# Kernel optimization log

Measured on AMD Instinct MI355X. Metric: run time of the kernel, lower is better.

## Reference

```python
import jax, jax.numpy as jnp
import numpy as np
from jax import lax

SIZES = [(159, 159), (159, 159), (79, 79), (79, 79), (39, 39), (19, 19), (19, 19), (19, 19)]
STRIDES = [4, 4, 8, 8, 16, 32, 32, 32]
RF_SIZES = [55.0, 71.0, 111.0, 143.0, 223.0, 383.0, 511.0, 639.0]
SCORE_THR = 0.35
IOU_THR = 0.5
MAX_BOXES = 100
BATCH = 32
CLS_C = 3  # class_num + 1


def _coords_fmap2orig(size, stride):
    h, w = size
    ys = (jnp.arange(h, dtype=jnp.float32) * stride + stride / 2.0)
    xs = (jnp.arange(w, dtype=jnp.float32) * stride + stride / 2.0)
    X, Y = jnp.meshgrid(xs, ys)  # row-major over (h, w)
    return jnp.stack([X.reshape(-1), Y.reshape(-1)], axis=-1)  # [h*w, 2]


def _flatten_cat(branches):
    # each branch [b,c,h,w] -> [b,h*w,c]; concat over anchors
    outs = [x.transpose(0, 2, 3, 1).reshape(x.shape[0], -1, x.shape[1]) for x in branches]
    return jnp.concatenate(outs, axis=1)


def _nms_keep(boxes, valid):
    # boxes [K,4] sorted by score desc, valid [K] bool. Greedy NMS, +1 area convention.
    x1, y1, x2, y2 = boxes[:, 0], boxes[:, 1], boxes[:, 2], boxes[:, 3]
    areas = (x2 - x1 + 1.0) * (y2 - y1 + 1.0)
    xmin = jnp.maximum(x1[:, None], x1[None, :])
    ymin = jnp.maximum(y1[:, None], y1[None, :])
    xmax = jnp.minimum(x2[:, None], x2[None, :])
    ymax = jnp.minimum(y2[:, None], y2[None, :])
    inter = jnp.clip(xmax - xmin, 0.0) * jnp.clip(ymax - ymin, 0.0)
    iou = inter / (areas[:, None] + areas[None, :] - inter)
    idx = jnp.arange(boxes.shape[0])

    def body(i, keep):
        sup = (iou[i] > IOU_THR) & (idx > i) & keep[i]
        return keep & ~sup

    return lax.fori_loop(0, boxes.shape[0], body, valid)


def setup_inputs() -> dict:
    key = jax.random.key(0)
    inp = {}
    ks = jax.random.split(key, 16)
    for i, (h, w) in enumerate(SIZES):
        inp[f"cls{i}"] = jax.random.normal(ks[i], (BATCH, CLS_C, h, w), dtype=jnp.float32)
        inp[f"reg{i}"] = jax.random.normal(ks[8 + i], (BATCH, 4, h, w), dtype=jnp.float32)
    return inp


def reference(cls0, cls1, cls2, cls3, cls4, cls5, cls6, cls7,
              reg0, reg1, reg2, reg3, reg4, reg5, reg6, reg7):
    cls_branches = [cls0, cls1, cls2, cls3, cls4, cls5, cls6, cls7]
    reg_branches = [reg0, reg1, reg2, reg3, reg4, reg5, reg6, reg7]

    cls_logits = _flatten_cat(cls_branches)   # [B, N, 3]
    reg_preds = _flatten_cat(reg_branches)    # [B, N, 4]
    coords = jnp.concatenate([_coords_fmap2orig(s, st) for s, st in zip(SIZES, STRIDES)], axis=0)  # [N,2]

    cls_preds = jax.nn.softmax(cls_logits, axis=2)
    cls_scores = jnp.max(cls_preds, axis=2)      # [B,N]
    cls_classes = jnp.argmax(cls_preds, axis=2)  # [B,N]

    rf_scale = jnp.concatenate([
        jnp.full((h * w,), rf / 2.0, dtype=jnp.float32) for (h, w), rf in zip(SIZES, RF_SIZES)
    ])  # [N]
    reg_preds = reg_preds * rf_scale[None, :, None]
    x1y1 = coords[None, :, :] - reg_preds[..., :2]
    x2y2 = coords[None, :, :] + reg_preds[..., 2:]
    boxes = jnp.concatenate([x1y1, x2y2], axis=2)  # [B,N,4]

    # foreground mask -> mask scores so topk picks fg first
    fg = cls_classes > 0
    masked_scores = jnp.where(fg, cls_scores, -1.0)
    top_scores, top_idx = lax.top_k(masked_scores, MAX_BOXES)  # [B,K], sorted desc
    top_boxes = jnp.take_along_axis(boxes, top_idx[..., None], axis=1)      # [B,K,4]
    top_classes = jnp.take_along_axis(cls_classes, top_idx, axis=1)         # [B,K]

    valid = (top_scores >= SCORE_THR) & (top_classes > 0)
    keep = jax.vmap(_nms_keep)(top_boxes, valid)  # [B,K] bool

    out_scores = jnp.where(keep, top_scores, 0.0)
    out_classes = jnp.where(keep, top_classes, 0)
    out_boxes = jnp.where(keep[..., None], top_boxes, 0.0)
    return out_scores, out_classes, out_boxes, keep
```

## Files before the change

kernel.cpp:

```cpp
#include <hip/hip_runtime.h>
#include <stdint.h>

#define N_ANCH 65648
#define NCHUNK 65
#define CHUNK  1024
#define NQ16   4103
#define CAP    2048
#define KBASE  0xBE800000u
#define NBATCH 32
#define TOPK   100
#define FT     1024

struct Ptrs { const float* cls[8]; const float* reg[8]; };

__constant__ int   c_off[9] = {0,25281,50562,56803,63044,64565,64926,65287,65648};
__constant__ int   c_sz[8]  = {159,159,79,79,39,19,19,19};
__constant__ float c_st[8]  = {4.f,4.f,8.f,8.f,16.f,32.f,32.f,32.f};
__constant__ float c_rf[8]  = {27.5f,35.5f,55.5f,71.5f,111.5f,191.5f,255.5f,319.5f};

__device__ inline uint32_t anchor_key(const Ptrs& p, int b, int n) {
  int k = 0;
#pragma unroll
  for (int q = 1; q < 8; ++q) if (n >= c_off[q]) k = q;
  int local = n - c_off[k];
  int hw = c_sz[k] * c_sz[k];
  const float* c = p.cls[k] + (size_t)(b * 3) * hw + local;
  float l0 = c[0], l1 = c[(size_t)hw], l2 = c[(size_t)2 * hw];
  float m = l0; int cl = 0;
  if (l1 > m) { m = l1; cl = 1; }
  if (l2 > m) { m = l2; cl = 2; }
  if (cl == 0) return 0u;
  float s = 1.0f / (expf(l0 - m) + expf(l1 - m) + expf(l2 - m));
  return __float_as_uint(s) | 0x80000000u;
}

__global__ __launch_bounds__(256) void k_bins(Ptrs p, uint8_t* bins, uint16_t* hist) {
  int bid = blockIdx.x;
  int b = bid / NCHUNK, chunk = bid % NCHUNK;
  int t = threadIdx.x;
  __shared__ uint32_t lh[256];
  lh[t] = 0;
  __syncthreads();
  int n0 = chunk * CHUNK + t * 4;
  if (n0 < N_ANCH) {
    uchar4 v; uint8_t* vb = (uint8_t*)&v;
#pragma unroll
    for (int u = 0; u < 4; ++u) {
      uint32_t key = anchor_key(p, b, n0 + u);
      uint8_t bin = key ? (uint8_t)((key - KBASE) >> 16) : (uint8_t)0;
      vb[u] = bin;
      if (bin) atomicAdd(&lh[bin], 1u);
    }
    *(uchar4*)(bins + (size_t)b * N_ANCH + n0) = v;
  }
  __syncthreads();
  hist[((size_t)b * NCHUNK + chunk) * 256 + t] = (uint16_t)lh[t];
}

template<int U>
__device__ inline void rank_select(const unsigned long long* s_all, int c, int c8, int t,
                                   unsigned long long* top) {
  unsigned long long mine[U]; int rk[U];
#pragma unroll
  for (int u = 0; u < U; ++u) {
    int i = t + u * FT;
    mine[u] = (i < c) ? s_all[i] : 0ull;
    rk[u] = 0;
  }
  for (int j = 0; j < c8; j += 8) {
    unsigned long long v0 = s_all[j+0], v1 = s_all[j+1], v2 = s_all[j+2], v3 = s_all[j+3];
    unsigned long long v4 = s_all[j+4], v5 = s_all[j+5], v6 = s_all[j+6], v7 = s_all[j+7];
#pragma unroll
    for (int u = 0; u < U; ++u) {
      rk[u] += (v0 > mine[u]) + (v1 > mine[u]) + (v2 > mine[u]) + (v3 > mine[u])
             + (v4 > mine[u]) + (v5 > mine[u]) + (v6 > mine[u]) + (v7 > mine[u]);
    }
  }
#pragma unroll
  for (int u = 0; u < U; ++u) {
    int i = t + u * FT;
    if (i < c && rk[u] < TOPK) top[rk[u]] = mine[u];
  }
}

__global__ __launch_bounds__(FT) void k_sel(Ptrs p, const uint8_t* bins,
                                            const uint16_t* hist, float* out) {
  int b = blockIdx.x, t = threadIdx.x;
  __shared__ uint32_t part[4][256];
  __shared__ uint32_t tot[256];
  __shared__ int s_idx[CAP];
  __shared__ unsigned long long s_all[CAP + 8];
  __shared__ unsigned long long top[TOPK];
  __shared__ float bx1[TOPK], by1[TOPK], bx2[TOPK], by2[TOPK], area[TOPK], sc[TOPK];
  __shared__ int cls_s[TOPK], keep[TOPK];
  __shared__ unsigned long long sup0[TOPK], sup1[TOPK];
  __shared__ unsigned long long s_km[2], s_km2[2];
  __shared__ uint32_t s_cnt;
  __shared__ int s_thr;

  {
    const uint16_t* hb = hist + (size_t)b * NCHUNK * 256;
    int g = t >> 8, tb = t & 255;
    uint32_t v0 = 0, v1 = 0, v2 = 0, v3 = 0;
    for (int ch = g; ch < NCHUNK; ch += 16) {
      v0 += hb[ch * 256 + tb];
      if (ch + 4 < NCHUNK)  v1 += hb[(ch + 4) * 256 + tb];
      if (ch + 8 < NCHUNK)  v2 += hb[(ch + 8) * 256 + tb];
      if (ch + 12 < NCHUNK) v3 += hb[(ch + 12) * 256 + tb];
    }
    part[g][tb] = v0 + v1 + v2 + v3;
    if (t == 0) s_cnt = 0;
    if (t < TOPK) top[t] = 0ull;
    __syncthreads();
    if (t < 256) tot[t] = part[0][t] + part[1][t] + part[2][t] + part[3][t];
    __syncthreads();
    for (int d = 1; d < 256; d <<= 1) {
      uint32_t add = 0;
      if (t < 256 && t + d < 256) add = tot[t + d];
      __syncthreads();
      if (t < 256) tot[t] += add;
      __syncthreads();
    }
    if (t < 256) {
      uint32_t suf = tot[t], sufn = (t < 255) ? tot[t + 1] : 0u;
      if (suf >= TOPK && sufn < TOPK) s_thr = t;
      if (t == 0 && tot[0] < TOPK) s_thr = 0;
    }
    __syncthreads();
  }
  int thr = s_thr; if (thr < 1) thr = 1;

  {
    const uint4* bp = (const uint4*)(bins + (size_t)b * N_ANCH);
    for (int i = t; i < NQ16; i += FT) {
      uint4 v4 = bp[i];
      uint32_t ws[4] = { v4.x, v4.y, v4.z, v4.w };
#pragma unroll
      for (int w = 0; w < 4; ++w) {
        uint32_t wv = ws[w];
        if (!wv) continue;
#pragma unroll
        for (int u = 0; u < 4; ++u) {
          int bin = (wv >> (8 * u)) & 0xFF;
          if (bin >= thr) {
            uint32_t q = atomicAdd(&s_cnt, 1u);
            if (q < CAP) s_idx[q] = i * 16 + w * 4 + u;
          }
        }
      }
    }
  }
  __syncthreads();
  int c = (int)min(s_cnt, (uint32_t)CAP);
  int c8 = (c + 7) & ~7;

  for (int i = t; i < c; i += FT) {
    int n = s_idx[i];
    s_all[i] = ((unsigned long long)anchor_key(p, b, n) << 32) | (uint32_t)(~(uint32_t)n);
  }
  for (int i = c + t; i < c8; i += FT) s_all[i] = 0ull;
  __syncthreads();

  if (c <= FT) rank_select<1>(s_all, c, c8, t, top);
  else         rank_select<2>(s_all, c, c8, t, top);
  __syncthreads();

  if (t < TOPK) {
    int r = t;
    unsigned long long pk = top[r];
    if (pk == 0ull) {
      sc[r] = -1.f; cls_s[r] = 0; keep[r] = 0;
      bx1[r] = by1[r] = bx2[r] = by2[r] = 0.f; area[r] = 1.f;
    } else {
      uint32_t key = (uint32_t)(pk >> 32);
      int n = (int)(~(uint32_t)pk);
      float score = __uint_as_float(key & 0x7FFFFFFFu);
      int k2 = 0;
#pragma unroll
      for (int q = 1; q < 8; ++q) if (n >= c_off[q]) k2 = q;
      int local = n - c_off[k2];
      int w = c_sz[k2], hw = w * w;
      int i2 = local / w, j2 = local % w;
      const float* cp = p.cls[k2] + (size_t)(b * 3) * hw + local;
      float l0 = cp[0], l1 = cp[(size_t)hw], l2 = cp[(size_t)2 * hw];
      float m = l0; int cl = 0;
      if (l1 > m) { m = l1; cl = 1; }
      if (l2 > m) { m = l2; cl = 2; }
      const float* rp = p.reg[k2] + (size_t)(b * 4) * hw + local;
      float r0 = rp[0], r1 = rp[(size_t)hw], r2 = rp[(size_t)2 * hw], r3 = rp[(size_t)3 * hw];
      float st = c_st[k2], rf = c_rf[k2];
      float cx = (float)j2 * st + st * 0.5f;
      float cy = (float)i2 * st + st * 0.5f;
      float x1 = cx - r0 * rf, y1 = cy - r1 * rf;
      float x2 = cx + r2 * rf, y2 = cy + r3 * rf;
      sc[r] = score; cls_s[r] = cl;
      bx1[r] = x1; by1[r] = y1; bx2[r] = x2; by2[r] = y2;
      area[r] = (x2 - x1 + 1.0f) * (y2 - y1 + 1.0f);
      keep[r] = (score >= 0.35f && cl > 0) ? 1 : 0;
    }
  }
  __syncthreads();

  if (t < TOPK) {
    float a1x = bx1[t], a1y = by1[t], a2x = bx2[t], a2y = by2[t], aA = area[t];
    unsigned long long m0 = 0, m1 = 0;
    for (int j = t + 1; j < TOPK; ++j) {
      float xmin = fmaxf(a1x, bx1[j]), ymin = fmaxf(a1y, by1[j]);
      float xmax = fminf(a2x, bx2[j]), ymax = fminf(a2y, by2[j]);
      float inter = fmaxf(xmax - xmin, 0.f) * fmaxf(ymax - ymin, 0.f);
      float iou = inter / (aA + area[j] - inter);
      if (iou > 0.5f) { if (j < 64) m0 |= 1ull << j; else m1 |= 1ull << (j - 64); }
    }
    sup0[t] = m0; sup1[t] = m1;
  }
  if (t < 64) {
    unsigned long long m = __ballot(keep[t] != 0);
    if (t == 0) s_km[0] = m;
  } else if (t < 128) {
    unsigned long long m = __ballot(t < TOPK && keep[t] != 0);
    if (t == 64) s_km[1] = m;
  }
  __syncthreads();

  if (t == 0) {
    unsigned long long km0 = s_km[0], km1 = s_km[1];
    for (int i0 = 0; i0 < TOPK; i0 += 8) {
      unsigned long long a0[8], a1[8];
#pragma unroll
      for (int q = 0; q < 8; ++q) {
        int i = i0 + q;
        a0[q] = (i < TOPK) ? sup0[i] : 0ull;
        a1[q] = (i < TOPK) ? sup1[i] : 0ull;
      }
#pragma unroll
      for (int q = 0; q < 8; ++q) {
        int i = i0 + q;
        if (i < TOPK) {
          bool ki = (i < 64) ? ((km0 >> i) & 1) : ((km1 >> (i - 64)) & 1);
          if (ki) { km0 &= ~a0[q]; km1 &= ~a1[q]; }
        }
      }
    }
    s_km2[0] = km0; s_km2[1] = km1;
  }
  __syncthreads();

  if (t < TOPK) {
    int r = t, o = b * TOPK + r;
    bool kp = (r < 64) ? ((s_km2[0] >> r) & 1) : ((s_km2[1] >> (r - 64)) & 1);
    out[o] = kp ? sc[r] : 0.f;
    out[NBATCH * TOPK + o] = kp ? (float)cls_s[r] : 0.f;
    float* ob = out + 2 * NBATCH * TOPK + (size_t)o * 4;
    ob[0] = kp ? bx1[r] : 0.f;
    ob[1] = kp ? by1[r] : 0.f;
    ob[2] = kp ? bx2[r] : 0.f;
    ob[3] = kp ? by2[r] : 0.f;
    out[6 * NBATCH * TOPK + o] = kp ? 1.f : 0.f;
  }
}

extern "C" void kernel_launch(void* const* d_in, const int* in_sizes, int n_in,
                              void* d_out, int out_size, void* d_ws, size_t ws_size,
                              hipStream_t stream) {
  Ptrs p;
  for (int i = 0; i < 8; ++i) {
    p.cls[i] = (const float*)d_in[2 * i];
    p.reg[i] = (const float*)d_in[2 * i + 1];
  }
  uint8_t*  bins = (uint8_t*)d_ws;
  uint16_t* hist = (uint16_t*)((char*)d_ws + 2100736);
  float* out = (float*)d_out;

  k_bins<<<NBATCH * NCHUNK, 256, 0, stream>>>(p, bins, hist);
  k_sel<<<NBATCH, FT, 0, stream>>>(p, bins, hist, out);
}
```

Measured before the change: 49.16 us.

## Split candidate collection into per-chunk kernel before per-batch merge

Moves the histogram threshold search, bin scan and candidate key computation out of the 32-block selection kernel into a new kernel launched with one block per (batch, chunk). Each block writes its candidates to a workspace segment, and a merge kernel prefix-sums the per-chunk counts and gathers the segments before rank selection and NMS. The intent is to spread the serial scan and the gather of candidate keys over 2080 blocks instead of 32. The cost is an extra launch, each block redoing the 65-chunk histogram reduction, and a round trip through global memory for the candidate keys.

```diff
diff --git a/kernel.cpp b/kernel.cpp
--- a/kernel.cpp
+++ b/kernel.cpp
@@ -4,12 +4,12 @@
 #define N_ANCH 65648
 #define NCHUNK 65
 #define CHUNK  1024
-#define NQ16   4103
+#define SEGCAP 1024
 #define CAP    2048
 #define KBASE  0xBE800000u
 #define NBATCH 32
 #define TOPK   100
-#define FT     1024
+#define MT     1024
 
 struct Ptrs { const float* cls[8]; const float* reg[8]; };
 
@@ -57,112 +57,113 @@
   hist[((size_t)b * NCHUNK + chunk) * 256 + t] = (uint16_t)lh[t];
 }
 
-template<int U>
-__device__ inline void rank_select(const unsigned long long* s_all, int c, int c8, int t,
-                                   unsigned long long* top) {
-  unsigned long long mine[U]; int rk[U];
-#pragma unroll
-  for (int u = 0; u < U; ++u) {
-    int i = t + u * FT;
-    mine[u] = (i < c) ? s_all[i] : 0ull;
-    rk[u] = 0;
-  }
-  for (int j = 0; j < c8; j += 8) {
-    unsigned long long v0 = s_all[j+0], v1 = s_all[j+1], v2 = s_all[j+2], v3 = s_all[j+3];
-    unsigned long long v4 = s_all[j+4], v5 = s_all[j+5], v6 = s_all[j+6], v7 = s_all[j+7];
-#pragma unroll
-    for (int u = 0; u < U; ++u) {
-      rk[u] += (v0 > mine[u]) + (v1 > mine[u]) + (v2 > mine[u]) + (v3 > mine[u])
-             + (v4 > mine[u]) + (v5 > mine[u]) + (v6 > mine[u]) + (v7 > mine[u]);
-    }
-  }
-#pragma unroll
-  for (int u = 0; u < U; ++u) {
-    int i = t + u * FT;
-    if (i < c && rk[u] < TOPK) top[rk[u]] = mine[u];
-  }
-}
-
-__global__ __launch_bounds__(FT) void k_sel(Ptrs p, const uint8_t* bins,
-                                            const uint16_t* hist, float* out) {
+__global__ __launch_bounds__(256) void k_collect(Ptrs p, const uint8_t* bins,
+                                                 const uint16_t* hist,
+                                                 unsigned long long* seg, uint32_t* cnt) {
+  int bid = blockIdx.x;
+  int b = bid / NCHUNK, chunk = bid % NCHUNK;
+  int t = threadIdx.x;
+  __shared__ uint32_t tot[256];
+  __shared__ int s_thr;
+  __shared__ uint32_t s_cnt;
+
+  const uint16_t* hb = hist + (size_t)b * NCHUNK * 256;
+  {
+    uint32_t v0 = 0, v1 = 0, v2 = 0, v3 = 0;
+    int ch = 0;
+    for (; ch + 4 <= NCHUNK; ch += 4) {
+      v0 += hb[(ch + 0) * 256 + t];
+      v1 += hb[(ch + 1) * 256 + t];
+      v2 += hb[(ch + 2) * 256 + t];
+      v3 += hb[(ch + 3) * 256 + t];
+    }
+    for (; ch < NCHUNK; ++ch) v0 += hb[ch * 256 + t];
+    tot[t] = v0 + v1 + v2 + v3;
+    if (t == 0) s_cnt = 0;
+    __syncthreads();
+    for (int d = 1; d < 256; d <<= 1) {
+      uint32_t add = (t + d < 256) ? tot[t + d] : 0u;
+      __syncthreads();
+      tot[t] += add;
+      __syncthreads();
+    }
+    uint32_t suf = tot[t], sufn = (t < 255) ? tot[t + 1] : 0u;
+    if (suf >= TOPK && sufn < TOPK) s_thr = t;
+    if (t == 0 && tot[0] < TOPK) s_thr = 0;
+    __syncthreads();
+  }
+  int thr = s_thr; if (thr < 1) thr = 1;
+
+  int n0 = chunk * CHUNK + t * 4;
+  unsigned long long* sg = seg + (size_t)bid * SEGCAP;
+  if (n0 < N_ANCH) {
+    uchar4 v4 = *(const uchar4*)(bins + (size_t)b * N_ANCH + n0);
+    const uint8_t* vb = (const uint8_t*)&v4;
+#pragma unroll
+    for (int u = 0; u < 4; ++u) {
+      if (vb[u] >= thr) {
+        uint32_t pos = atomicAdd(&s_cnt, 1u);
+        int n = n0 + u;
+        sg[pos] = ((unsigned long long)anchor_key(p, b, n) << 32) |
+                  (uint32_t)(~(uint32_t)n);
+      }
+    }
+  }
+  __syncthreads();
+  if (t == 0) cnt[bid] = s_cnt;
+}
+
+__global__ __launch_bounds__(MT) void k_merge(Ptrs p, const uint32_t* cnt,
+                                              const unsigned long long* seg, float* out) {
   int b = blockIdx.x, t = threadIdx.x;
-  __shared__ uint32_t part[4][256];
-  __shared__ uint32_t tot[256];
-  __shared__ int s_idx[CAP];
+  __shared__ uint32_t pref[NCHUNK + 1];
   __shared__ unsigned long long s_all[CAP + 8];
   __shared__ unsigned long long top[TOPK];
   __shared__ float bx1[TOPK], by1[TOPK], bx2[TOPK], by2[TOPK], area[TOPK], sc[TOPK];
   __shared__ int cls_s[TOPK], keep[TOPK];
   __shared__ unsigned long long sup0[TOPK], sup1[TOPK];
   __shared__ unsigned long long s_km[2], s_km2[2];
-  __shared__ uint32_t s_cnt;
-  __shared__ int s_thr;
+
+  if (t < NCHUNK) pref[t + 1] = cnt[b * NCHUNK + t];
+  if (t == 0) pref[0] = 0;
+  if (t < TOPK) top[t] = 0ull;
+  __syncthreads();
+  for (int d = 1; d < NCHUNK + 1; d <<= 1) {
+    uint32_t v = 0;
+    if (t < NCHUNK + 1 && t >= d) v = pref[t - d];
+    __syncthreads();
+    if (t < NCHUNK + 1) pref[t] += v;
+    __syncthreads();
+  }
+  int c = (int)min(pref[NCHUNK], (uint32_t)CAP);
+  int c8 = (c + 7) & ~7;
+
+  for (int i = t; i < c; i += MT) {
+    int lo = 0, hi = NCHUNK - 1;
+    while (lo < hi) {
+      int mid = (lo + hi + 1) >> 1;
+      if ((int)pref[mid] <= i) lo = mid; else hi = mid - 1;
+    }
+    s_all[i] = seg[((size_t)b * NCHUNK + lo) * SEGCAP + (i - (int)pref[lo])];
+  }
+  for (int i = c + t; i < c8; i += MT) s_all[i] = 0ull;
+  __syncthreads();
 
   {
-    const uint16_t* hb = hist + (size_t)b * NCHUNK * 256;
-    int g = t >> 8, tb = t & 255;
-    uint32_t v0 = 0, v1 = 0, v2 = 0, v3 = 0;
-    for (int ch = g; ch < NCHUNK; ch += 16) {
-      v0 += hb[ch * 256 + tb];
-      if (ch + 4 < NCHUNK)  v1 += hb[(ch + 4) * 256 + tb];
-      if (ch + 8 < NCHUNK)  v2 += hb[(ch + 8) * 256 + tb];
-      if (ch + 12 < NCHUNK) v3 += hb[(ch + 12) * 256 + tb];
-    }
-    part[g][tb] = v0 + v1 + v2 + v3;
-    if (t == 0) s_cnt = 0;
-    if (t < TOPK) top[t] = 0ull;
-    __syncthreads();
-    if (t < 256) tot[t] = part[0][t] + part[1][t] + part[2][t] + part[3][t];
-    __syncthreads();
-    for (int d = 1; d < 256; d <<= 1) {
-      uint32_t add = 0;
-      if (t < 256 && t + d < 256) add = tot[t + d];
-      __syncthreads();
-      if (t < 256) tot[t] += add;
-      __syncthreads();
-    }
-    if (t < 256) {
-      uint32_t suf = tot[t], sufn = (t < 255) ? tot[t + 1] : 0u;
-      if (suf >= TOPK && sufn < TOPK) s_thr = t;
-      if (t == 0 && tot[0] < TOPK) s_thr = 0;
-    }
-    __syncthreads();
-  }
-  int thr = s_thr; if (thr < 1) thr = 1;
-
-  {
-    const uint4* bp = (const uint4*)(bins + (size_t)b * N_ANCH);
-    for (int i = t; i < NQ16; i += FT) {
-      uint4 v4 = bp[i];
-      uint32_t ws[4] = { v4.x, v4.y, v4.z, v4.w };
-#pragma unroll
-      for (int w = 0; w < 4; ++w) {
-        uint32_t wv = ws[w];
-        if (!wv) continue;
-#pragma unroll
-        for (int u = 0; u < 4; ++u) {
-          int bin = (wv >> (8 * u)) & 0xFF;
-          if (bin >= thr) {
-            uint32_t q = atomicAdd(&s_cnt, 1u);
-            if (q < CAP) s_idx[q] = i * 16 + w * 4 + u;
-          }
-        }
-      }
-    }
-  }
-  __syncthreads();
-  int c = (int)min(s_cnt, (uint32_t)CAP);
-  int c8 = (c + 7) & ~7;
-
-  for (int i = t; i < c; i += FT) {
-    int n = s_idx[i];
-    s_all[i] = ((unsigned long long)anchor_key(p, b, n) << 32) | (uint32_t)(~(uint32_t)n);
-  }
-  for (int i = c + t; i < c8; i += FT) s_all[i] = 0ull;
-  __syncthreads();
-
-  if (c <= FT) rank_select<1>(s_all, c, c8, t, top);
-  else         rank_select<2>(s_all, c, c8, t, top);
+    unsigned long long m0 = (t < c) ? s_all[t] : 0ull;
+    unsigned long long m1 = (t + MT < c) ? s_all[t + MT] : 0ull;
+    int r0 = 0, r1 = 0;
+    for (int j = 0; j < c8; j += 8) {
+      unsigned long long v0 = s_all[j+0], v1 = s_all[j+1], v2 = s_all[j+2], v3 = s_all[j+3];
+      unsigned long long v4 = s_all[j+4], v5 = s_all[j+5], v6 = s_all[j+6], v7 = s_all[j+7];
+      r0 += (v0 > m0) + (v1 > m0) + (v2 > m0) + (v3 > m0)
+          + (v4 > m0) + (v5 > m0) + (v6 > m0) + (v7 > m0);
+      r1 += (v0 > m1) + (v1 > m1) + (v2 > m1) + (v3 > m1)
+          + (v4 > m1) + (v5 > m1) + (v6 > m1) + (v7 > m1);
+    }
+    if (m0 && r0 < TOPK) top[r0] = m0;
+    if (m1 && r1 < TOPK) top[r1] = m1;
+  }
   __syncthreads();
 
   if (t < TOPK) {
@@ -269,8 +270,12 @@
   }
   uint8_t*  bins = (uint8_t*)d_ws;
   uint16_t* hist = (uint16_t*)((char*)d_ws + 2100736);
+  uint32_t* cnt  = (uint32_t*)((char*)d_ws + 3165696);
+  unsigned long long* seg =
+      (unsigned long long*)((char*)d_ws + 3174016);
   float* out = (float*)d_out;
 
   k_bins<<<NBATCH * NCHUNK, 256, 0, stream>>>(p, bins, hist);
-  k_sel<<<NBATCH, FT, 0, stream>>>(p, bins, hist, out);
-}
+  k_collect<<<NBATCH * NCHUNK, 256, 0, stream>>>(p, bins, hist, seg, cnt);
+  k_merge<<<NBATCH, MT, 0, stream>>>(p, cnt, seg, out);
+}
```

Measured after the change: 57.12 us. 1.16x slower.

## Prefetch bins early, fuse key build into compaction, warp-scan threshold

Applied to the files above, without the earlier changes.

The select kernel now loads its batch's packed bin bytes into registers before the histogram reduction, so that global load overlaps the prefix-sum work. The 8-step block-wide suffix scan with many barriers becomes a single-wavefront shuffle scan. Candidate keys are computed directly during compaction, which removes the s_idx array, one pass and one barrier. The rank selection always handles two items per thread instead of branching on count. In exchange, register pressure rises and the gathers of anchor keys now happen under the atomic append.

```diff
diff --git a/kernel.cpp b/kernel.cpp
--- a/kernel.cpp
+++ b/kernel.cpp
@@ -57,39 +57,12 @@
   hist[((size_t)b * NCHUNK + chunk) * 256 + t] = (uint16_t)lh[t];
 }
 
-template<int U>
-__device__ inline void rank_select(const unsigned long long* s_all, int c, int c8, int t,
-                                   unsigned long long* top) {
-  unsigned long long mine[U]; int rk[U];
-#pragma unroll
-  for (int u = 0; u < U; ++u) {
-    int i = t + u * FT;
-    mine[u] = (i < c) ? s_all[i] : 0ull;
-    rk[u] = 0;
-  }
-  for (int j = 0; j < c8; j += 8) {
-    unsigned long long v0 = s_all[j+0], v1 = s_all[j+1], v2 = s_all[j+2], v3 = s_all[j+3];
-    unsigned long long v4 = s_all[j+4], v5 = s_all[j+5], v6 = s_all[j+6], v7 = s_all[j+7];
-#pragma unroll
-    for (int u = 0; u < U; ++u) {
-      rk[u] += (v0 > mine[u]) + (v1 > mine[u]) + (v2 > mine[u]) + (v3 > mine[u])
-             + (v4 > mine[u]) + (v5 > mine[u]) + (v6 > mine[u]) + (v7 > mine[u]);
-    }
-  }
-#pragma unroll
-  for (int u = 0; u < U; ++u) {
-    int i = t + u * FT;
-    if (i < c && rk[u] < TOPK) top[rk[u]] = mine[u];
-  }
-}
-
 __global__ __launch_bounds__(FT) void k_sel(Ptrs p, const uint8_t* bins,
                                             const uint16_t* hist, float* out) {
   int b = blockIdx.x, t = threadIdx.x;
   __shared__ uint32_t part[4][256];
   __shared__ uint32_t tot[256];
-  __shared__ int s_idx[CAP];
-  __shared__ unsigned long long s_all[CAP + 8];
+  __shared__ unsigned long long s_all[CAP];
   __shared__ unsigned long long top[TOPK];
   __shared__ float bx1[TOPK], by1[TOPK], bx2[TOPK], by2[TOPK], area[TOPK], sc[TOPK];
   __shared__ int cls_s[TOPK], keep[TOPK];
@@ -97,6 +70,18 @@
   __shared__ unsigned long long s_km[2], s_km2[2];
   __shared__ uint32_t s_cnt;
   __shared__ int s_thr;
+
+  const uint4* bp = (const uint4*)(bins + (size_t)b * N_ANCH);
+  uint4 bq0 = bp[t];
+  uint4 bq1 = bp[1024 + t];
+  uint4 bq2 = bp[2048 + t];
+  uint4 bq3 = bp[3072 + t];
+  uint4 bq4 = make_uint4(0, 0, 0, 0);
+  if (t < 7) bq4 = bp[4096 + t];
+
+  for (int i = t; i < CAP; i += FT) s_all[i] = 0ull;
+  if (t < TOPK) top[t] = 0ull;
+  if (t == 0) s_cnt = 0;
 
   {
     const uint16_t* hb = hist + (size_t)b * NCHUNK * 256;
@@ -109,42 +94,57 @@
       if (ch + 12 < NCHUNK) v3 += hb[(ch + 12) * 256 + tb];
     }
     part[g][tb] = v0 + v1 + v2 + v3;
-    if (t == 0) s_cnt = 0;
-    if (t < TOPK) top[t] = 0ull;
-    __syncthreads();
-    if (t < 256) tot[t] = part[0][t] + part[1][t] + part[2][t] + part[3][t];
-    __syncthreads();
-    for (int d = 1; d < 256; d <<= 1) {
-      uint32_t add = 0;
-      if (t < 256 && t + d < 256) add = tot[t + d];
-      __syncthreads();
-      if (t < 256) tot[t] += add;
-      __syncthreads();
-    }
-    if (t < 256) {
-      uint32_t suf = tot[t], sufn = (t < 255) ? tot[t + 1] : 0u;
-      if (suf >= TOPK && sufn < TOPK) s_thr = t;
-      if (t == 0 && tot[0] < TOPK) s_thr = 0;
-    }
-    __syncthreads();
-  }
-  int thr = s_thr; if (thr < 1) thr = 1;
+  }
+  __syncthreads();
+  if (t < 256) tot[t] = part[0][t] + part[1][t] + part[2][t] + part[3][t];
+  __syncthreads();
+
+  if (t < 64) {
+    int l = t;
+    uint32_t t0 = tot[4 * l], t1 = tot[4 * l + 1], t2 = tot[4 * l + 2], t3 = tot[4 * l + 3];
+    uint32_t s = t0 + t1 + t2 + t3;
+    uint32_t S = s;
+#pragma unroll
+    for (int off = 1; off < 64; off <<= 1) {
+      uint32_t v = __shfl_down(S, off);
+      if (l + off < 64) S += v;
+    }
+    uint32_t total = __shfl(S, 0);
+    uint32_t E = S - s;
+    uint32_t suf3 = t3 + E;
+    uint32_t suf2 = t2 + suf3;
+    uint32_t suf1 = t1 + suf2;
+    uint32_t suf0 = S;
+    if (total < TOPK) { if (l == 0) s_thr = 0; }
+    else {
+      if (suf0 >= TOPK && suf1 < TOPK) s_thr = 4 * l + 0;
+      if (suf1 >= TOPK && suf2 < TOPK) s_thr = 4 * l + 1;
+      if (suf2 >= TOPK && suf3 < TOPK) s_thr = 4 * l + 2;
+      if (suf3 >= TOPK && E    < TOPK) s_thr = 4 * l + 3;
+    }
+  }
+  __syncthreads();
+  uint32_t thr = (uint32_t)max(s_thr, 1);
 
   {
-    const uint4* bp = (const uint4*)(bins + (size_t)b * N_ANCH);
-    for (int i = t; i < NQ16; i += FT) {
-      uint4 v4 = bp[i];
-      uint32_t ws[4] = { v4.x, v4.y, v4.z, v4.w };
+    uint4 qs[5] = { bq0, bq1, bq2, bq3, bq4 };
+    int qidx[5] = { t, 1024 + t, 2048 + t, 3072 + t, 4096 + t };
+#pragma unroll
+    for (int z = 0; z < 5; ++z) {
+      if (z == 4 && t >= 7) break;
+      uint32_t ws[4] = { qs[z].x, qs[z].y, qs[z].z, qs[z].w };
 #pragma unroll
       for (int w = 0; w < 4; ++w) {
         uint32_t wv = ws[w];
         if (!wv) continue;
 #pragma unroll
         for (int u = 0; u < 4; ++u) {
-          int bin = (wv >> (8 * u)) & 0xFF;
-          if (bin >= thr) {
+          if (((wv >> (8 * u)) & 0xFFu) >= thr) {
+            int n = qidx[z] * 16 + w * 4 + u;
             uint32_t q = atomicAdd(&s_cnt, 1u);
-            if (q < CAP) s_idx[q] = i * 16 + w * 4 + u;
+            if (q < CAP)
+              s_all[q] = ((unsigned long long)anchor_key(p, b, n) << 32) |
+                         (uint32_t)(~(uint32_t)n);
           }
         }
       }
@@ -154,15 +154,21 @@
   int c = (int)min(s_cnt, (uint32_t)CAP);
   int c8 = (c + 7) & ~7;
 
-  for (int i = t; i < c; i += FT) {
-    int n = s_idx[i];
-    s_all[i] = ((unsigned long long)anchor_key(p, b, n) << 32) | (uint32_t)(~(uint32_t)n);
-  }
-  for (int i = c + t; i < c8; i += FT) s_all[i] = 0ull;
-  __syncthreads();
-
-  if (c <= FT) rank_select<1>(s_all, c, c8, t, top);
-  else         rank_select<2>(s_all, c, c8, t, top);
+  {
+    unsigned long long m0 = (t < c) ? s_all[t] : 0ull;
+    unsigned long long m1 = (t + FT < c) ? s_all[t + FT] : 0ull;
+    int r0 = 0, r1 = 0;
+    for (int j = 0; j < c8; j += 8) {
+      unsigned long long v0 = s_all[j+0], v1 = s_all[j+1], v2 = s_all[j+2], v3 = s_all[j+3];
+      unsigned long long v4 = s_all[j+4], v5 = s_all[j+5], v6 = s_all[j+6], v7 = s_all[j+7];
+      r0 += (v0 > m0) + (v1 > m0) + (v2 > m0) + (v3 > m0)
+          + (v4 > m0) + (v5 > m0) + (v6 > m0) + (v7 > m0);
+      r1 += (v0 > m1) + (v1 > m1) + (v2 > m1) + (v3 > m1)
+          + (v4 > m1) + (v5 > m1) + (v6 > m1) + (v7 > m1);
+    }
+    if (m0 && r0 < TOPK) top[r0] = m0;
+    if (m1 && r1 < TOPK) top[r1] = m1;
+  }
   __syncthreads();
 
   if (t < TOPK) {
```

After: 59.93 us. +21.9%, slower.
